# Kernel tuning notes

Hardware: AMD Instinct MI355X
Metric: run time of the kernel (lower is better)

Reference implementation:

```python
import jax, jax.numpy as jnp
import numpy as np

B, S, D = 2, 4096, 512
H = 8
W = 512            # local attention window size
HD = D // H        # head dim
NC = S // W        # number of chunks
HALF = W // 2      # symmetric half-window


def setup_inputs() -> dict:
    key = jax.random.key(0)
    ks = jax.random.split(key, 12)
    s = 1.0 / np.sqrt(D)
    return {
        "val": jax.random.normal(ks[0], (B, S, D), jnp.float32),
        "Wq": jax.random.normal(ks[1], (D, D), jnp.float32) * s,
        "bq": jnp.zeros((D,), jnp.float32),
        "Wk": jax.random.normal(ks[2], (D, D), jnp.float32) * s,
        "bk": jnp.zeros((D,), jnp.float32),
        "Wv": jax.random.normal(ks[3], (D, D), jnp.float32) * s,
        "bv": jnp.zeros((D,), jnp.float32),
        "Wo": jax.random.normal(ks[4], (D, D), jnp.float32) * s,
        "bo": jnp.zeros((D,), jnp.float32),
        "gamma": jnp.ones((D,), jnp.float32),
        "beta": jnp.zeros((D,), jnp.float32),
    }


def _heads(x):
    # [B,S,D] -> [B,H,S,HD]
    return x.reshape(B, S, H, HD).transpose(0, 2, 1, 3)


def _gather_neighbors(x):
    # x: [B,H,S,HD] -> [B,H,NC,3W,HD] (prev | cur | next chunk, zero-padded at ends)
    xp = jnp.pad(x, ((0, 0), (0, 0), (W, W), (0, 0)))
    xc = xp.reshape(B, H, NC + 2, W, HD)
    return jnp.concatenate([xc[:, :, :-2], xc[:, :, 1:-1], xc[:, :, 2:]], axis=3)


def _local_attention(x, Wq, bq, Wk, bk, Wv, bv, Wo, bo):
    q = _heads(x @ Wq + bq)
    k = _heads(x @ Wk + bk)
    v = _heads(x @ Wv + bv)

    qc = q.reshape(B, H, NC, W, HD)            # chunked queries
    kn = _gather_neighbors(k)                  # [B,H,NC,3W,HD]
    vn = _gather_neighbors(v)

    scale = 1.0 / np.sqrt(HD)
    scores = jnp.einsum("bhcqd,bhckd->bhcqk", qc, kn) * scale  # [B,H,NC,W,3W]

    # banded mask: key relative position in [-HALF, HALF], and key index in [0,S)
    qi = jnp.arange(W)[:, None]
    kj = jnp.arange(3 * W)[None, :]
    band = jnp.abs(kj - W - qi) <= HALF                          # [W,3W]
    key_pos = (jnp.arange(NC)[:, None, None] - 1) * W + kj[None]  # [NC,1,3W]
    valid = (key_pos >= 0) & (key_pos < S)                       # [NC,1,3W]
    mask = band[None] & valid                                    # [NC,W,3W]

    scores = jnp.where(mask[None, None], scores, jnp.float32(-1e9))
    p = jax.nn.softmax(scores, axis=-1)
    o = jnp.einsum("bhcqk,bhckd->bhcqd", p, vn)                  # [B,H,NC,W,HD]
    o = o.reshape(B, H, S, HD).transpose(0, 2, 1, 3).reshape(B, S, D)
    return o @ Wo + bo


def _layer_norm(x, gamma, beta, eps=1e-5):
    mu = jnp.mean(x, axis=-1, keepdims=True)
    var = jnp.mean(jnp.square(x - mu), axis=-1, keepdims=True)
    return (x - mu) * jax.lax.rsqrt(var + eps) * gamma + beta


def reference(val, Wq, bq, Wk, bk, Wv, bv, Wo, bo, gamma, beta):
    attn_out = _local_attention(val, Wq, bq, Wk, bk, Wv, bv, Wo, bo)
    return _layer_norm(val + attn_out, gamma, beta)
```

## Files before the change

### kernel.cpp

```cpp
#include <hip/hip_runtime.h>
#include <hip/hip_bf16.h>

#define BATCH 2
#define SEQ   4096
#define DIM   512
#define NHEAD 8
#define HDIM  64
#define ROWS  (BATCH*SEQ)

typedef float  fx4   __attribute__((ext_vector_type(4)));
typedef __bf16 bf16x8 __attribute__((ext_vector_type(8)));
typedef unsigned short ushort_t;
typedef unsigned short usx4 __attribute__((ext_vector_type(4)));
typedef unsigned short usx8 __attribute__((ext_vector_type(8)));

static __device__ __forceinline__ float b2f(ushort_t v) {
    union { unsigned int u; float f; } c; c.u = ((unsigned int)v) << 16; return c.f;
}
static __device__ __forceinline__ ushort_t f2b(float f) {
    union { float f; unsigned int u; } c; c.f = f;
    unsigned int u = c.u;
    unsigned int r = (u + 0x7FFFu + ((u >> 16) & 1u)) >> 16;
    return (ushort_t)r;
}
static __device__ __forceinline__ void gload16(const ushort_t* g, ushort_t* l) {
    __builtin_amdgcn_global_load_lds(
        (const __attribute__((address_space(1))) unsigned int*)g,
        (__attribute__((address_space(3))) unsigned int*)l, 16, 0, 0);
}

__global__ __launch_bounds__(256) void prep_kernel(
    const float* __restrict__ val, ushort_t* __restrict__ xb,
    const float* __restrict__ W0, const float* __restrict__ W1,
    const float* __restrict__ W2, const float* __restrict__ W3,
    ushort_t* __restrict__ T0, ushort_t* __restrict__ T1,
    ushort_t* __restrict__ T2, ushort_t* __restrict__ T3) {

    const int tid = threadIdx.x;
    if (blockIdx.y == 4) {
        const int stride = 64 * 256 * 4;
        for (int i = (blockIdx.x * 256 + tid) * 4; i < ROWS * 512; i += stride) {
            fx4 v = *(const fx4*)(val + i);
            usx4 o; o.x = f2b(v.x); o.y = f2b(v.y); o.z = f2b(v.z); o.w = f2b(v.w);
            *(usx4*)(xb + i) = o;
        }
        return;
    }
    const float* W; ushort_t* WT;
    switch (blockIdx.y) {
        case 0: W = W0; WT = T0; break;
        case 1: W = W1; WT = T1; break;
        case 2: W = W2; WT = T2; break;
        default: W = W3; WT = T3; break;
    }
    __shared__ float tile[64][65];
    int r0 = (blockIdx.x & 7) * 64;
    int c0 = (blockIdx.x >> 3) * 64;
    for (int idx = tid; idx < 4096; idx += 256) {
        int rr = idx >> 6, cc = idx & 63;
        tile[rr][cc] = W[(c0 + rr) * 512 + (r0 + cc)];
    }
    __syncthreads();
    for (int idx = tid; idx < 4096; idx += 256) {
        int rr = idx >> 6, cc = idx & 63;
        WT[(size_t)(r0 + rr) * 512 + (c0 + cc)] = f2b(tile[cc][rr]);
    }
}

__global__ __launch_bounds__(256) void gemm128_kernel(
    const ushort_t* __restrict__ A,
    const ushort_t* __restrict__ BT0, const ushort_t* __restrict__ BT1, const ushort_t* __restrict__ BT2,
    const float* __restrict__ b0, const float* __restrict__ b1, const float* __restrict__ b2,
    ushort_t* __restrict__ C0, ushort_t* __restrict__ C1, ushort_t* __restrict__ C2) {

    const ushort_t* BT; const float* bias; ushort_t* C;
    if (blockIdx.z == 0)      { BT = BT0; bias = b0; C = C0; }
    else if (blockIdx.z == 1) { BT = BT1; bias = b1; C = C1; }
    else                      { BT = BT2; bias = b2; C = C2; }

    __shared__ ushort_t As[2][128 * 32];
    __shared__ ushort_t Bs[2][128 * 32];

    const int tid  = threadIdx.x;
    const int wave = tid >> 6;
    const int lane = tid & 63;
    const int lm   = lane & 15;
    const int quad = lane >> 4;
    const int wm   = wave >> 1;
    const int wn   = wave & 1;

    const int m0t = blockIdx.x * 128;
    const int n0t = blockIdx.y * 128;

    const int srow = tid >> 2, sgc = tid & 3;
    const ushort_t* ga0 = A  + (size_t)(m0t + srow) * 512 + sgc * 8;
    const ushort_t* ga1 = ga0 + (size_t)64 * 512;
    const ushort_t* gb0 = BT + (size_t)(n0t + srow) * 512 + sgc * 8;
    const ushort_t* gb1 = gb0 + (size_t)64 * 512;

    const int aoff = (wm * 64 + lm) * 32 + quad * 8;
    const int boff = (wn * 64 + lm) * 32 + quad * 8;

    fx4 acc[4][4];
    #pragma unroll
    for (int i = 0; i < 4; ++i)
        #pragma unroll
        for (int j = 0; j < 4; ++j) acc[i][j] = 0;

    gload16(ga0, &As[0][tid * 8]);
    gload16(ga1, &As[0][(tid + 256) * 8]);
    gload16(gb0, &Bs[0][tid * 8]);
    gload16(gb1, &Bs[0][(tid + 256) * 8]);

    for (int it = 0; it < 16; ++it) {
        const int cur = it & 1, nxt = cur ^ 1;
        __syncthreads();
        if (it < 15) {
            const int k0 = (it + 1) * 32;
            gload16(ga0 + k0, &As[nxt][tid * 8]);
            gload16(ga1 + k0, &As[nxt][(tid + 256) * 8]);
            gload16(gb0 + k0, &Bs[nxt][tid * 8]);
            gload16(gb1 + k0, &Bs[nxt][(tid + 256) * 8]);
        }
        bf16x8 af[4], bfr[4];
        #pragma unroll
        for (int ms = 0; ms < 4; ++ms) af[ms]  = *(const bf16x8*)&As[cur][aoff + ms * 512];
        #pragma unroll
        for (int ns = 0; ns < 4; ++ns) bfr[ns] = *(const bf16x8*)&Bs[cur][boff + ns * 512];
        #pragma unroll
        for (int ms = 0; ms < 4; ++ms)
            #pragma unroll
            for (int ns = 0; ns < 4; ++ns)
                acc[ms][ns] = __builtin_amdgcn_mfma_f32_16x16x32_bf16(af[ms], bfr[ns], acc[ms][ns], 0, 0, 0);
    }

    const int crow0 = m0t + wm * 64 + quad * 4;
    const int ccol0 = n0t + wn * 64 + lm;

    if (blockIdx.z == 2) {
        #pragma unroll
        for (int ns = 0; ns < 4; ++ns) {
            int col = ccol0 + ns * 16;
            int h = col >> 6, d = col & 63;
            float bv = bias[col];
            #pragma unroll
            for (int ms = 0; ms < 4; ++ms) {
                int m = crow0 + ms * 16;
                int bb = m >> 12, s0 = m & 4095;
                usx4 o;
                o.x = f2b(acc[ms][ns][0] + bv); o.y = f2b(acc[ms][ns][1] + bv);
                o.z = f2b(acc[ms][ns][2] + bv); o.w = f2b(acc[ms][ns][3] + bv);
                *(usx4*)(C + (((size_t)(bb * 8 + h) * 64 + d) * 4096 + s0)) = o;
            }
        }
    } else {
        #pragma unroll
        for (int ns = 0; ns < 4; ++ns) {
            int col = ccol0 + ns * 16;
            float bv = bias[col];
            #pragma unroll
            for (int ms = 0; ms < 4; ++ms) {
                #pragma unroll
                for (int r = 0; r < 4; ++r) {
                    C[(size_t)(crow0 + ms * 16 + r) * 512 + col] = f2b(acc[ms][ns][r] + bv);
                }
            }
        }
    }
}

__global__ __launch_bounds__(256) void attn_mfma_kernel(
    const ushort_t* __restrict__ Qb, const ushort_t* __restrict__ Kb,
    const ushort_t* __restrict__ Vt, ushort_t* __restrict__ Ob) {

    __shared__ ushort_t Klds[64 * 64];
    __shared__ ushort_t Vlds[64 * 64];
    __shared__ ushort_t Plds[4 * 32 * 72];

    const int tid  = threadIdx.x;
    const int wave = tid >> 6;
    const int lane = tid & 63;
    const int lm   = lane & 15;
    const int quad = lane >> 4;

    const int bh = blockIdx.y;
    const int b = bh >> 3, h = bh & 7;
    const int q0 = blockIdx.x * 128;
    const int qw = q0 + wave * 32;

    bf16x8 qf[2][2];
    #pragma unroll
    for (int qs = 0; qs < 2; ++qs) {
        const ushort_t* qp = Qb + ((size_t)(b * SEQ + qw + qs * 16 + lm)) * 512 + h * 64 + quad * 8;
        qf[qs][0] = *(const bf16x8*)qp;
        qf[qs][1] = *(const bf16x8*)(qp + 32);
    }

    int koff[2][4], voff[2][4];
    #pragma unroll
    for (int ks = 0; ks < 2; ++ks) {
        #pragma unroll
        for (int tn = 0; tn < 4; ++tn) {
            int key = tn * 16 + lm;
            koff[ks][tn] = key * 64 + (((ks * 4 + quad) ^ (key & 7)) * 8);
            int d = tn * 16 + lm;
            voff[ks][tn] = d * 64 + (((ks * 4 + quad) ^ (d & 7)) * 8);
        }
    }
    ushort_t* Pw = Plds + wave * (32 * 72);
    int pread[2][2];
    #pragma unroll
    for (int qs = 0; qs < 2; ++qs)
        #pragma unroll
        for (int ks = 0; ks < 2; ++ks)
            pread[qs][ks] = (qs * 16 + lm) * 72 + ks * 32 + quad * 8;

    const int skey = tid >> 3;
    const int sdg  = tid & 7;
    const size_t kgbase = ((size_t)b * SEQ) * 512 + h * 64 + sdg * 8;
    const size_t vgbase = ((size_t)bh * 64) * 4096 + sdg * 8;
    const int l0 = skey * 64 + ((sdg ^ (skey & 7)) * 8);
    const int l1 = l0 + 32 * 64;

    const int klo = (q0 >= 256) ? 0 : ((256 - q0) >> 6);
    const int khi = min(9, (4288 - q0) >> 6);
    const int wlo = wave >> 1, whi = 8 + (wave >> 1);
    const int flo = 1 + (wave >> 1), fhi = 7 + (wave >> 1);

    bf16x8 onesf;
    {
        __bf16 o = (lm == 0) ? (__bf16)1.0f : (__bf16)0.0f;
        #pragma unroll
        for (int j = 0; j < 8; ++j) onesf[j] = o;
    }

    fx4 oacc[2][4];
    #pragma unroll
    for (int qs = 0; qs < 2; ++qs)
        #pragma unroll
        for (int tn = 0; tn < 4; ++tn) oacc[qs][tn] = 0;
    fx4 lacc[2];
    lacc[0] = 0; lacc[1] = 0;

    usx8 kn0, kn1, vn0, vn1;
    {
        int ts = q0 - 256 + klo * 64;
        kn0 = *(const usx8*)(Kb + kgbase + (size_t)(ts + skey) * 512);
        kn1 = *(const usx8*)(Kb + kgbase + (size_t)(ts + skey + 32) * 512);
        vn0 = *(const usx8*)(Vt + vgbase + (size_t)skey * 4096 + ts);
        vn1 = *(const usx8*)(Vt + vgbase + (size_t)(skey + 32) * 4096 + ts);
    }

    for (int kt = klo; kt <= khi; ++kt) {
        const int ts = q0 - 256 + kt * 64;
        __syncthreads();
        *(usx8*)&Klds[l0] = kn0;
        *(usx8*)&Klds[l1] = kn1;
        *(usx8*)&Vlds[l0] = vn0;
        *(usx8*)&Vlds[l1] = vn1;
        __syncthreads();

        if (kt < khi) {
            int t2 = ts + 64;
            kn0 = *(const usx8*)(Kb + kgbase + (size_t)(t2 + skey) * 512);
            kn1 = *(const usx8*)(Kb + kgbase + (size_t)(t2 + skey + 32) * 512);
            vn0 = *(const usx8*)(Vt + vgbase + (size_t)skey * 4096 + t2);
            vn1 = *(const usx8*)(Vt + vgbase + (size_t)(skey + 32) * 4096 + t2);
        }

        if (kt < wlo || kt > whi) continue;

        bf16x8 kf[2][4];
        #pragma unroll
        for (int ks = 0; ks < 2; ++ks)
            #pragma unroll
            for (int tn = 0; tn < 4; ++tn)
                kf[ks][tn] = *(const bf16x8*)&Klds[koff[ks][tn]];
        fx4 sacc[2][4];
        #pragma unroll
        for (int qs = 0; qs < 2; ++qs)
            #pragma unroll
            for (int tn = 0; tn < 4; ++tn) sacc[qs][tn] = 0;
        #pragma unroll
        for (int ks = 0; ks < 2; ++ks)
            #pragma unroll
            for (int tn = 0; tn < 4; ++tn) {
                sacc[0][tn] = __builtin_amdgcn_mfma_f32_16x16x32_bf16(qf[0][ks], kf[ks][tn], sacc[0][tn], 0, 0, 0);
                sacc[1][tn] = __builtin_amdgcn_mfma_f32_16x16x32_bf16(qf[1][ks], kf[ks][tn], sacc[1][tn], 0, 0, 0);
            }

        const bool edge = (kt < flo) || (kt > fhi);
        #pragma unroll
        for (int qs = 0; qs < 2; ++qs) {
            #pragma unroll
            for (int tn = 0; tn < 4; ++tn) {
                int kg = ts + tn * 16 + lm;
                #pragma unroll
                for (int r = 0; r < 4; ++r) {
                    float p = __expf(sacc[qs][tn][r] * 0.125f);
                    if (edge) {
                        int dlt = kg - (qw + qs * 16 + quad * 4 + r);
                        p = (dlt <= 256 && dlt >= -256) ? p : 0.0f;
                    }
                    Pw[(qs * 16 + quad * 4 + r) * 72 + tn * 16 + lm] = f2b(p);
                }
            }
        }

        bf16x8 vf[2][4];
        #pragma unroll
        for (int ks = 0; ks < 2; ++ks)
            #pragma unroll
            for (int tn = 0; tn < 4; ++tn)
                vf[ks][tn] = *(const bf16x8*)&Vlds[voff[ks][tn]];
        #pragma unroll
        for (int qs = 0; qs < 2; ++qs) {
            #pragma unroll
            for (int ks = 0; ks < 2; ++ks) {
                bf16x8 ap = *(const bf16x8*)&Pw[pread[qs][ks]];
                lacc[qs] = __builtin_amdgcn_mfma_f32_16x16x32_bf16(ap, onesf, lacc[qs], 0, 0, 0);
                #pragma unroll
                for (int tn = 0; tn < 4; ++tn)
                    oacc[qs][tn] = __builtin_amdgcn_mfma_f32_16x16x32_bf16(ap, vf[ks][tn], oacc[qs][tn], 0, 0, 0);
            }
        }
    }

    #pragma unroll
    for (int qs = 0; qs < 2; ++qs) {
        float linv[4];
        #pragma unroll
        for (int r = 0; r < 4; ++r) {
            float lv = __shfl(lacc[qs][r], (lane & 48));
            linv[r] = 1.0f / lv;
        }
        ushort_t* ob = Ob + ((size_t)(b * SEQ + qw + qs * 16 + quad * 4)) * 512 + h * 64 + lm;
        #pragma unroll
        for (int tn = 0; tn < 4; ++tn)
            #pragma unroll
            for (int r = 0; r < 4; ++r)
                ob[(size_t)r * 512 + tn * 16] = f2b(oacc[qs][tn][r] * linv[r]);
    }
}

__global__ __launch_bounds__(256) void ln_kernel(
    const ushort_t* __restrict__ xb, const ushort_t* __restrict__ ob,
    const float* __restrict__ gamma, const float* __restrict__ beta,
    float* __restrict__ out) {

    int row  = blockIdx.x * 4 + (threadIdx.x >> 6);
    int lane = threadIdx.x & 63;

    const ushort_t* xp = xb + (size_t)row * 512 + lane * 8;
    const ushort_t* op = ob + (size_t)row * 512 + lane * 8;

    usx4 xa = ((const usx4*)xp)[0];
    usx4 xc = ((const usx4*)xp)[1];
    usx4 oa = ((const usx4*)op)[0];
    usx4 oc = ((const usx4*)op)[1];
    fx4 va, vb;
    va.x = b2f(xa.x) + b2f(oa.x); va.y = b2f(xa.y) + b2f(oa.y);
    va.z = b2f(xa.z) + b2f(oa.z); va.w = b2f(xa.w) + b2f(oa.w);
    vb.x = b2f(xc.x) + b2f(oc.x); vb.y = b2f(xc.y) + b2f(oc.y);
    vb.z = b2f(xc.z) + b2f(oc.z); vb.w = b2f(xc.w) + b2f(oc.w);

    float s = va.x + va.y + va.z + va.w + vb.x + vb.y + vb.z + vb.w;
    #pragma unroll
    for (int m = 32; m > 0; m >>= 1) s += __shfl_xor(s, m);
    float mu = s * (1.0f / 512.0f);

    fx4 da = va - mu;
    fx4 db = vb - mu;
    float ss = da.x*da.x + da.y*da.y + da.z*da.z + da.w*da.w
             + db.x*db.x + db.y*db.y + db.z*db.z + db.w*db.w;
    #pragma unroll
    for (int m = 32; m > 0; m >>= 1) ss += __shfl_xor(ss, m);
    float rstd = rsqrtf(ss * (1.0f / 512.0f) + 1e-5f);

    const fx4* gp = (const fx4*)(gamma + lane * 8);
    const fx4* bp = (const fx4*)(beta  + lane * 8);
    fx4 g0 = gp[0], g1 = gp[1], b0 = bp[0], b1 = bp[1];

    float* outp = out + (size_t)row * 512 + lane * 8;
    fx4 r0 = da * rstd * g0 + b0;
    fx4 r1 = db * rstd * g1 + b1;
    ((fx4*)outp)[0] = r0;
    ((fx4*)outp)[1] = r1;
}

extern "C" void kernel_launch(void* const* d_in, const int* in_sizes, int n_in,
                              void* d_out, int out_size, void* d_ws, size_t ws_size,
                              hipStream_t stream) {
    const float* val   = (const float*)d_in[0];
    const float* Wq    = (const float*)d_in[1];
    const float* bq    = (const float*)d_in[2];
    const float* Wk    = (const float*)d_in[3];
    const float* bk    = (const float*)d_in[4];
    const float* Wv    = (const float*)d_in[5];
    const float* bv    = (const float*)d_in[6];
    const float* Wo    = (const float*)d_in[7];
    const float* bo    = (const float*)d_in[8];
    const float* gamma = (const float*)d_in[9];
    const float* beta  = (const float*)d_in[10];
    float* out = (float*)d_out;

    char* w = (char*)d_ws;
    ushort_t* xb    = (ushort_t*)w; w += (size_t)ROWS * 512 * 2;
    ushort_t* WqT   = (ushort_t*)w; w += 512 * 512 * 2;
    ushort_t* WkT   = (ushort_t*)w; w += 512 * 512 * 2;
    ushort_t* WvT   = (ushort_t*)w; w += 512 * 512 * 2;
    ushort_t* WoT   = (ushort_t*)w; w += 512 * 512 * 2;
    ushort_t* Qb    = (ushort_t*)w; w += (size_t)ROWS * 512 * 2;
    ushort_t* Kb    = (ushort_t*)w; w += (size_t)ROWS * 512 * 2;
    ushort_t* Vtb   = (ushort_t*)w; w += (size_t)ROWS * 512 * 2;
    ushort_t* attnb = (ushort_t*)w; w += (size_t)ROWS * 512 * 2;
    ushort_t* obuf  = (ushort_t*)w; w += (size_t)ROWS * 512 * 2;

    prep_kernel<<<dim3(64, 5), 256, 0, stream>>>(
        val, xb, Wq, Wk, Wv, Wo, WqT, WkT, WvT, WoT);

    gemm128_kernel<<<dim3(ROWS / 128, 4, 3), 256, 0, stream>>>(
        xb, WqT, WkT, WvT, bq, bk, bv, Qb, Kb, Vtb);

    attn_mfma_kernel<<<dim3(SEQ / 128, BATCH * NHEAD), 256, 0, stream>>>(Qb, Kb, Vtb, attnb);

    gemm128_kernel<<<dim3(ROWS / 128, 4, 1), 256, 0, stream>>>(
        attnb, WoT, WoT, WoT, bo, bo, bo, obuf, obuf, obuf);

    ln_kernel<<<ROWS / 4, 256, 0, stream>>>(xb, obuf, gamma, beta, out);
}
```

Before: 182.5 us.

## Shrink attention query tile, single-buffer GEMM LDS, widen prep conversion grid

```diff
diff --git a/kernel.cpp b/kernel.cpp
--- a/kernel.cpp
+++ b/kernel.cpp
@@ -37,9 +37,10 @@
     ushort_t* __restrict__ T2, ushort_t* __restrict__ T3) {
 
     const int tid = threadIdx.x;
-    if (blockIdx.y == 4) {
-        const int stride = 64 * 256 * 4;
-        for (int i = (blockIdx.x * 256 + tid) * 4; i < ROWS * 512; i += stride) {
+    if (blockIdx.y >= 4) {
+        const int bid = blockIdx.x + 64 * (blockIdx.y - 4);
+        const int stride = 256 * 256 * 4;
+        for (int i = (bid * 256 + tid) * 4; i < ROWS * 512; i += stride) {
             fx4 v = *(const fx4*)(val + i);
             usx4 o; o.x = f2b(v.x); o.y = f2b(v.y); o.z = f2b(v.z); o.w = f2b(v.w);
             *(usx4*)(xb + i) = o;
@@ -78,8 +79,8 @@
     else if (blockIdx.z == 1) { BT = BT1; bias = b1; C = C1; }
     else                      { BT = BT2; bias = b2; C = C2; }
 
-    __shared__ ushort_t As[2][128 * 32];
-    __shared__ ushort_t Bs[2][128 * 32];
+    __shared__ ushort_t As[128 * 32];
+    __shared__ ushort_t Bs[128 * 32];
 
     const int tid  = threadIdx.x;
     const int wave = tid >> 6;
@@ -97,6 +98,10 @@
     const ushort_t* ga1 = ga0 + (size_t)64 * 512;
     const ushort_t* gb0 = BT + (size_t)(n0t + srow) * 512 + sgc * 8;
     const ushort_t* gb1 = gb0 + (size_t)64 * 512;
+    ushort_t* la0 = As + tid * 8;
+    ushort_t* la1 = As + (tid + 256) * 8;
+    ushort_t* lb0 = Bs + tid * 8;
+    ushort_t* lb1 = Bs + (tid + 256) * 8;
 
     const int aoff = (wm * 64 + lm) * 32 + quad * 8;
     const int boff = (wn * 64 + lm) * 32 + quad * 8;
@@ -107,26 +112,19 @@
         #pragma unroll
         for (int j = 0; j < 4; ++j) acc[i][j] = 0;
 
-    gload16(ga0, &As[0][tid * 8]);
-    gload16(ga1, &As[0][(tid + 256) * 8]);
-    gload16(gb0, &Bs[0][tid * 8]);
-    gload16(gb1, &Bs[0][(tid + 256) * 8]);
-
-    for (int it = 0; it < 16; ++it) {
-        const int cur = it & 1, nxt = cur ^ 1;
+    for (int k0 = 0; k0 < 512; k0 += 32) {
         __syncthreads();
-        if (it < 15) {
-            const int k0 = (it + 1) * 32;
-            gload16(ga0 + k0, &As[nxt][tid * 8]);
-            gload16(ga1 + k0, &As[nxt][(tid + 256) * 8]);
-            gload16(gb0 + k0, &Bs[nxt][tid * 8]);
-            gload16(gb1 + k0, &Bs[nxt][(tid + 256) * 8]);
-        }
+        gload16(ga0 + k0, la0);
+        gload16(ga1 + k0, la1);
+        gload16(gb0 + k0, lb0);
+        gload16(gb1 + k0, lb1);
+        __syncthreads();
+
         bf16x8 af[4], bfr[4];
         #pragma unroll
-        for (int ms = 0; ms < 4; ++ms) af[ms]  = *(const bf16x8*)&As[cur][aoff + ms * 512];
-        #pragma unroll
-        for (int ns = 0; ns < 4; ++ns) bfr[ns] = *(const bf16x8*)&Bs[cur][boff + ns * 512];
+        for (int ms = 0; ms < 4; ++ms) af[ms]  = *(const bf16x8*)&As[aoff + ms * 512];
+        #pragma unroll
+        for (int ns = 0; ns < 4; ++ns) bfr[ns] = *(const bf16x8*)&Bs[boff + ns * 512];
         #pragma unroll
         for (int ms = 0; ms < 4; ++ms)
             #pragma unroll
@@ -169,13 +167,13 @@
     }
 }
 
-__global__ __launch_bounds__(256) void attn_mfma_kernel(
+__global__ __launch_bounds__(256, 4) void attn_mfma_kernel(
     const ushort_t* __restrict__ Qb, const ushort_t* __restrict__ Kb,
     const ushort_t* __restrict__ Vt, ushort_t* __restrict__ Ob) {
 
     __shared__ ushort_t Klds[64 * 64];
     __shared__ ushort_t Vlds[64 * 64];
-    __shared__ ushort_t Plds[4 * 32 * 72];
+    __shared__ ushort_t Plds[4 * 16 * 72];
 
     const int tid  = threadIdx.x;
     const int wave = tid >> 6;
@@ -185,16 +183,12 @@
 
     const int bh = blockIdx.y;
     const int b = bh >> 3, h = bh & 7;
-    const int q0 = blockIdx.x * 128;
-    const int qw = q0 + wave * 32;
-
-    bf16x8 qf[2][2];
-    #pragma unroll
-    for (int qs = 0; qs < 2; ++qs) {
-        const ushort_t* qp = Qb + ((size_t)(b * SEQ + qw + qs * 16 + lm)) * 512 + h * 64 + quad * 8;
-        qf[qs][0] = *(const bf16x8*)qp;
-        qf[qs][1] = *(const bf16x8*)(qp + 32);
-    }
+    const int q0 = blockIdx.x * 64;
+    const int qw = q0 + wave * 16;
+
+    const ushort_t* qp = Qb + ((size_t)(b * SEQ + qw + lm)) * 512 + h * 64 + quad * 8;
+    bf16x8 qf0 = *(const bf16x8*)qp;
+    bf16x8 qf1 = *(const bf16x8*)(qp + 32);
 
     int koff[2][4], voff[2][4];
     #pragma unroll
@@ -207,13 +201,9 @@
             voff[ks][tn] = d * 64 + (((ks * 4 + quad) ^ (d & 7)) * 8);
         }
     }
-    ushort_t* Pw = Plds + wave * (32 * 72);
-    int pread[2][2];
-    #pragma unroll
-    for (int qs = 0; qs < 2; ++qs)
-        #pragma unroll
-        for (int ks = 0; ks < 2; ++ks)
-            pread[qs][ks] = (qs * 16 + lm) * 72 + ks * 32 + quad * 8;
+    ushort_t* Pw = Plds + wave * (16 * 72);
+    const int pwbase = lm * 72 + quad * 4;
+    const int prbase = lm * 72 + quad * 8;
 
     const int skey = tid >> 3;
     const int sdg  = tid & 7;
@@ -223,9 +213,7 @@
     const int l1 = l0 + 32 * 64;
 
     const int klo = (q0 >= 256) ? 0 : ((256 - q0) >> 6);
-    const int khi = min(9, (4288 - q0) >> 6);
-    const int wlo = wave >> 1, whi = 8 + (wave >> 1);
-    const int flo = 1 + (wave >> 1), fhi = 7 + (wave >> 1);
+    const int khi = min(8, (4288 - q0) >> 6);
 
     bf16x8 onesf;
     {
@@ -234,13 +222,9 @@
         for (int j = 0; j < 8; ++j) onesf[j] = o;
     }
 
-    fx4 oacc[2][4];
-    #pragma unroll
-    for (int qs = 0; qs < 2; ++qs)
-        #pragma unroll
-        for (int tn = 0; tn < 4; ++tn) oacc[qs][tn] = 0;
-    fx4 lacc[2];
-    lacc[0] = 0; lacc[1] = 0;
+    fx4 oacc[4];
+    oacc[0] = 0; oacc[1] = 0; oacc[2] = 0; oacc[3] = 0;
+    fx4 lacc = 0;
 
     usx8 kn0, kn1, vn0, vn1;
     {
@@ -268,43 +252,37 @@
             vn1 = *(const usx8*)(Vt + vgbase + (size_t)(skey + 32) * 4096 + t2);
         }
 
-        if (kt < wlo || kt > whi) continue;
-
         bf16x8 kf[2][4];
         #pragma unroll
         for (int ks = 0; ks < 2; ++ks)
             #pragma unroll
             for (int tn = 0; tn < 4; ++tn)
                 kf[ks][tn] = *(const bf16x8*)&Klds[koff[ks][tn]];
-        fx4 sacc[2][4];
-        #pragma unroll
-        for (int qs = 0; qs < 2; ++qs)
-            #pragma unroll
-            for (int tn = 0; tn < 4; ++tn) sacc[qs][tn] = 0;
-        #pragma unroll
-        for (int ks = 0; ks < 2; ++ks)
-            #pragma unroll
-            for (int tn = 0; tn < 4; ++tn) {
-                sacc[0][tn] = __builtin_amdgcn_mfma_f32_16x16x32_bf16(qf[0][ks], kf[ks][tn], sacc[0][tn], 0, 0, 0);
-                sacc[1][tn] = __builtin_amdgcn_mfma_f32_16x16x32_bf16(qf[1][ks], kf[ks][tn], sacc[1][tn], 0, 0, 0);
+        fx4 sacc[4];
+        sacc[0] = 0; sacc[1] = 0; sacc[2] = 0; sacc[3] = 0;
+        #pragma unroll
+        for (int ks = 0; ks < 2; ++ks) {
+            bf16x8 q8 = ks ? qf1 : qf0;
+            #pragma unroll
+            for (int tn = 0; tn < 4; ++tn)
+                sacc[tn] = __builtin_amdgcn_mfma_f32_16x16x32_bf16(kf[ks][tn], q8, sacc[tn], 0, 0, 0);
+        }
+
+        const bool edge = (ts < qw - 241) || (ts > qw + 193);
+        const int qg = qw + lm;
+        #pragma unroll
+        for (int tn = 0; tn < 4; ++tn) {
+            usx4 pk;
+            #pragma unroll
+            for (int r = 0; r < 4; ++r) {
+                float p = __expf(sacc[tn][r] * 0.125f);
+                if (edge) {
+                    int dlt = (ts + tn * 16 + quad * 4 + r) - qg;
+                    p = (dlt <= 256 && dlt >= -256) ? p : 0.0f;
+                }
+                pk[r] = f2b(p);
             }
-
-        const bool edge = (kt < flo) || (kt > fhi);
-        #pragma unroll
-        for (int qs = 0; qs < 2; ++qs) {
-            #pragma unroll
-            for (int tn = 0; tn < 4; ++tn) {
-                int kg = ts + tn * 16 + lm;
-                #pragma unroll
-                for (int r = 0; r < 4; ++r) {
-                    float p = __expf(sacc[qs][tn][r] * 0.125f);
-                    if (edge) {
-                        int dlt = kg - (qw + qs * 16 + quad * 4 + r);
-                        p = (dlt <= 256 && dlt >= -256) ? p : 0.0f;
-                    }
-                    Pw[(qs * 16 + quad * 4 + r) * 72 + tn * 16 + lm] = f2b(p);
-                }
-            }
+            *(usx4*)&Pw[pwbase + tn * 16] = pk;
         }
 
         bf16x8 vf[2][4];
@@ -314,33 +292,27 @@
             for (int tn = 0; tn < 4; ++tn)
                 vf[ks][tn] = *(const bf16x8*)&Vlds[voff[ks][tn]];
         #pragma unroll
-        for (int qs = 0; qs < 2; ++qs) {
-            #pragma unroll
-            for (int ks = 0; ks < 2; ++ks) {
-                bf16x8 ap = *(const bf16x8*)&Pw[pread[qs][ks]];
-                lacc[qs] = __builtin_amdgcn_mfma_f32_16x16x32_bf16(ap, onesf, lacc[qs], 0, 0, 0);
-                #pragma unroll
-                for (int tn = 0; tn < 4; ++tn)
-                    oacc[qs][tn] = __builtin_amdgcn_mfma_f32_16x16x32_bf16(ap, vf[ks][tn], oacc[qs][tn], 0, 0, 0);
-            }
-        }
-    }
-
-    #pragma unroll
-    for (int qs = 0; qs < 2; ++qs) {
-        float linv[4];
-        #pragma unroll
-        for (int r = 0; r < 4; ++r) {
-            float lv = __shfl(lacc[qs][r], (lane & 48));
-            linv[r] = 1.0f / lv;
-        }
-        ushort_t* ob = Ob + ((size_t)(b * SEQ + qw + qs * 16 + quad * 4)) * 512 + h * 64 + lm;
-        #pragma unroll
-        for (int tn = 0; tn < 4; ++tn)
-            #pragma unroll
-            for (int r = 0; r < 4; ++r)
-                ob[(size_t)r * 512 + tn * 16] = f2b(oacc[qs][tn][r] * linv[r]);
-    }
+        for (int ks = 0; ks < 2; ++ks) {
+            bf16x8 ap = *(const bf16x8*)&Pw[prbase + ks * 32];
+            lacc = __builtin_amdgcn_mfma_f32_16x16x32_bf16(ap, onesf, lacc, 0, 0, 0);
+            #pragma unroll
+            for (int tn = 0; tn < 4; ++tn)
+                oacc[tn] = __builtin_amdgcn_mfma_f32_16x16x32_bf16(ap, vf[ks][tn], oacc[tn], 0, 0, 0);
+        }
+    }
+
+    float linv[4];
+    #pragma unroll
+    for (int r = 0; r < 4; ++r) {
+        float lv = __shfl(lacc[r], (lane & 48));
+        linv[r] = 1.0f / lv;
+    }
+    ushort_t* ob = Ob + ((size_t)(b * SEQ + qw + quad * 4)) * 512 + h * 64 + lm;
+    #pragma unroll
+    for (int tn = 0; tn < 4; ++tn)
+        #pragma unroll
+        for (int r = 0; r < 4; ++r)
+            ob[(size_t)r * 512 + tn * 16] = f2b(oacc[tn][r] * linv[r]);
 }
 
 __global__ __launch_bounds__(256) void ln_kernel(
@@ -416,13 +388,13 @@
     ushort_t* attnb = (ushort_t*)w; w += (size_t)ROWS * 512 * 2;
     ushort_t* obuf  = (ushort_t*)w; w += (size_t)ROWS * 512 * 2;
 
-    prep_kernel<<<dim3(64, 5), 256, 0, stream>>>(
+    prep_kernel<<<dim3(64, 8), 256, 0, stream>>>(
         val, xb, Wq, Wk, Wv, Wo, WqT, WkT, WvT, WoT);
 
     gemm128_kernel<<<dim3(ROWS / 128, 4, 3), 256, 0, stream>>>(
         xb, WqT, WkT, WvT, bq, bk, bv, Qb, Kb, Vtb);
 
-    attn_mfma_kernel<<<dim3(SEQ / 128, BATCH * NHEAD), 256, 0, stream>>>(Qb, Kb, Vtb, attnb);
+    attn_mfma_kernel<<<dim3(SEQ / 64, BATCH * NHEAD), 256, 0, stream>>>(Qb, Kb, Vtb, attnb);
 
     gemm128_kernel<<<dim3(ROWS / 128, 4, 1), 256, 0, stream>>>(
         attnb, WoT, WoT, WoT, bo, bo, bo, obuf, obuf, obuf);
```

Measured after the change: 165.3 us. 9.4% less time.
